# Performance work log

Measured on AMD Instinct MI355X. Metric: run time of the kernel, lower is better.

## Reference

```python
import jax, jax.numpy as jnp
import numpy as np

BSZ, L, D = 8, 2048, 1024

def setup_inputs() -> dict:
    key = jax.random.key(0)
    k1, k2, k3, k4 = jax.random.split(key, 4)
    s = 1.0 / np.sqrt(D)
    return {
        "x":   jax.random.normal(k1, (BSZ, L, D), dtype=jnp.float32),
        "A":   jax.random.normal(k2, (D,), dtype=jnp.float32),
        "W_B": jax.random.normal(k3, (D, D), dtype=jnp.float32) * s,
        "b_B": jnp.zeros((D,), dtype=jnp.float32),
        "W_C": jax.random.normal(k4, (D, D), dtype=jnp.float32) * s,
        "b_C": jnp.zeros((D,), dtype=jnp.float32),
    }

def reference(x, A, W_B, b_B, W_C, b_C):
    # Precompute B(x_t) for all t in one GEMM: [B, L, D]
    Bx = jnp.einsum("bld,ed->ble", x, W_B) + b_B
    h0 = jnp.zeros((x.shape[0], x.shape[2]), dtype=x.dtype)

    def step(h, bx_t):
        h = jnp.tanh(A * h + bx_t)   # elementwise recurrence
        return h, h

    # scan over time: Bx -> [L, B, D]
    _, hs = jax.lax.scan(step, h0, jnp.swapaxes(Bx, 0, 1))
    # y_t = C(h_t), batched over all t: hs [L, B, D]
    y = jnp.einsum("lbd,ed->lbe", hs, W_C) + b_C
    return jnp.swapaxes(y, 0, 1)  # [B, L, D]
```

## Files before the change

### kernel.cpp

```cpp
#include <hip/hip_runtime.h>
#include <hip/hip_bf16.h>
#include <stdint.h>


using short8 = __attribute__((ext_vector_type(8))) short;
using f32x4  = __attribute__((ext_vector_type(4))) float;

#define DEV __device__ __forceinline__

DEV ushort f2bf_rn(float x) {
  uint32_t u = __float_as_uint(x);
  uint32_t r = (u + 0x7FFFu + ((u >> 16) & 1u)) >> 16;
  return (ushort)r;
}
DEV float bf2f(ushort b) { return __uint_as_float(((uint32_t)b) << 16); }

DEV void gload_lds16(const void* g, void* l) {
  __builtin_amdgcn_global_load_lds((const __attribute__((address_space(1))) void*)g,
                                   (__attribute__((address_space(3))) void*)l,
                                   16, 0, 0);
}

__global__ void k_split_convert(const float* __restrict__ in, ushort* __restrict__ hi,
                                ushort* __restrict__ lo, int n4) {
  const int stride = gridDim.x * blockDim.x;
  for (int i = blockIdx.x * blockDim.x + threadIdx.x; i < n4; i += stride) {
    float4 v = reinterpret_cast<const float4*>(in)[i];
    ushort4 hv, lv;
    hv.x = f2bf_rn(v.x); lv.x = f2bf_rn(v.x - bf2f(hv.x));
    hv.y = f2bf_rn(v.y); lv.y = f2bf_rn(v.y - bf2f(hv.y));
    hv.z = f2bf_rn(v.z); lv.z = f2bf_rn(v.z - bf2f(hv.z));
    hv.w = f2bf_rn(v.w); lv.w = f2bf_rn(v.w - bf2f(hv.w));
    reinterpret_cast<ushort4*>(hi)[i] = hv;
    reinterpret_cast<ushort4*>(lo)[i] = lv;
  }
}

__global__ void k_convert(const float* __restrict__ in, ushort* __restrict__ hi, int n4) {
  const int stride = gridDim.x * blockDim.x;
  for (int i = blockIdx.x * blockDim.x + threadIdx.x; i < n4; i += stride) {
    float4 v = reinterpret_cast<const float4*>(in)[i];
    ushort4 hv;
    hv.x = f2bf_rn(v.x); hv.y = f2bf_rn(v.y);
    hv.z = f2bf_rn(v.z); hv.w = f2bf_rn(v.w);
    reinterpret_cast<ushort4*>(hi)[i] = hv;
  }
}

template <int SPLIT>
__global__ __launch_bounds__(256, 2)
void k_gemm_bt(const ushort* __restrict__ Ah, const ushort* __restrict__ Al,
               const ushort* __restrict__ Bh, const ushort* __restrict__ Bl,
               const float* __restrict__ bias, float* __restrict__ C,
               int M, int N, int K) {
  constexpr int NMAT = SPLIT ? 4 : 2;
  __shared__ __align__(1024) ushort lds[NMAT * 128 * 64];
  ushort* sAh = lds;
  ushort* sAl = lds + (SPLIT ? 8192 : 0);
  ushort* sBh = lds + (SPLIT ? 16384 : 8192);
  ushort* sBl = lds + (SPLIT ? 24576 : 8192);

  const int t = threadIdx.x;
  const int lane = t & 63;
  const int w = t >> 6;
  const int wm = w >> 1, wn = w & 1;
  const int bm = blockIdx.y, bn = blockIdx.x;
  const int lr = lane & 15;
  const int lk = (lane >> 4) << 3;

  const ushort* gA_h = Ah + (size_t)(bm * 128) * K;
  const ushort* gA_l = SPLIT ? (Al + (size_t)(bm * 128) * K) : gA_h;
  const ushort* gB_h = Bh + (size_t)(bn * 128) * K;
  const ushort* gB_l = SPLIT ? (Bl + (size_t)(bn * 128) * K) : gB_h;

  f32x4 acc[4][4];
#pragma unroll
  for (int i = 0; i < 4; ++i)
#pragma unroll
    for (int j = 0; j < 4; ++j)
#pragma unroll
      for (int r = 0; r < 4; ++r) acc[i][j][r] = 0.f;

  auto stage = [&](int kt) {
    const int k0 = kt * 64;
#pragma unroll
    for (int i = 0; i < 4; ++i) {
      const int lin16 = i * 256 + t;
      const int lb = lin16 << 4;
      const int row = lb >> 7;
      const int srcb = (lb & 127) ^ ((row & 7) << 4);
      const size_t goff = (size_t)row * K + (size_t)(k0 + (srcb >> 1));
      const int lidx = i * 2048 + w * 512;
      gload_lds16(gA_h + goff, sAh + lidx);
      if (SPLIT) gload_lds16(gA_l + goff, sAl + lidx);
      gload_lds16(gB_h + goff, sBh + lidx);
      if (SPLIT) gload_lds16(gB_l + goff, sBl + lidx);
    }
  };

  auto ldfrag = [&](const ushort* s, int row, int kc) -> short8 {
    const int byte = (row << 7) + (((kc << 1) ^ ((row & 7) << 4)));
    return *reinterpret_cast<const short8*>(reinterpret_cast<const char*>(s) + byte);
  };

  const int NT = K / 64;
  stage(0);
  for (int kt = 0; kt < NT; ++kt) {
    __syncthreads();
#pragma unroll
    for (int kk = 0; kk < 2; ++kk) {
      short8 ah[4], bh[4], al[4], bl[4];
      const int kc = kk * 32 + lk;
#pragma unroll
      for (int i = 0; i < 4; ++i) {
        const int row = wm * 64 + i * 16 + lr;
        ah[i] = ldfrag(sAh, row, kc);
        if (SPLIT) al[i] = ldfrag(sAl, row, kc);
      }
#pragma unroll
      for (int j = 0; j < 4; ++j) {
        const int row = wn * 64 + j * 16 + lr;
        bh[j] = ldfrag(sBh, row, kc);
        if (SPLIT) bl[j] = ldfrag(sBl, row, kc);
      }
#pragma unroll
      for (int i = 0; i < 4; ++i)
#pragma unroll
        for (int j = 0; j < 4; ++j) {
          acc[i][j] = __builtin_amdgcn_mfma_f32_16x16x32_bf16(ah[i], bh[j], acc[i][j], 0, 0, 0);
          if (SPLIT) {
            acc[i][j] = __builtin_amdgcn_mfma_f32_16x16x32_bf16(al[i], bh[j], acc[i][j], 0, 0, 0);
            acc[i][j] = __builtin_amdgcn_mfma_f32_16x16x32_bf16(ah[i], bl[j], acc[i][j], 0, 0, 0);
          }
        }
    }
    __syncthreads();
    if (kt + 1 < NT) stage(kt + 1);
  }

  float* Cb = C + (size_t)(bm * 128) * N + bn * 128;
#pragma unroll
  for (int i = 0; i < 4; ++i)
#pragma unroll
    for (int j = 0; j < 4; ++j) {
      const int col = wn * 64 + j * 16 + lr;
      const float bv = bias[bn * 128 + col];
#pragma unroll
      for (int r = 0; r < 4; ++r) {
        const int rowt = wm * 64 + i * 16 + ((lane >> 4) << 2) + r;
        Cb[(size_t)rowt * N + col] = acc[i][j][r] + bv;
      }
    }
}

__global__ __launch_bounds__(64)
void k_recurrence(const float* __restrict__ Bx, const float* __restrict__ Avec,
                  ushort* __restrict__ Hout) {
  const int tid = blockIdx.x * 64 + threadIdx.x;
  const int b = tid >> 10;
  const int d = tid & 1023;
  const float a = Avec[d];
  const float* bx = Bx + (size_t)b * 2048 * 1024 + d;
  ushort* ho = Hout + (size_t)b * 2048 * 1024 + d;

  constexpr int P = 32;
  constexpr int NC = 2048 / P;
  float buf[P];
#pragma unroll
  for (int i = 0; i < P; ++i) buf[i] = bx[(size_t)i * 1024];
  float h = 0.f;
  for (int c = 0; c < NC; ++c) {
    float nbuf[P];
    if (c + 1 < NC) {
#pragma unroll
      for (int i = 0; i < P; ++i) nbuf[i] = bx[(size_t)((c + 1) * P + i) * 1024];
    } else {
#pragma unroll
      for (int i = 0; i < P; ++i) nbuf[i] = 0.f;
    }
#pragma unroll
    for (int i = 0; i < P; ++i) {
      float u = fmaf(a, h, buf[i]);
      u = fminf(15.f, fmaxf(-15.f, u));
      const float p = __expf(u + u);
      h = (p - 1.f) * __builtin_amdgcn_rcpf(p + 1.f);
      ho[(size_t)(c * P + i) * 1024] = f2bf_rn(h);
    }
#pragma unroll
    for (int i = 0; i < P; ++i) buf[i] = nbuf[i];
  }
}

extern "C" void kernel_launch(void* const* d_in, const int* in_sizes, int n_in,
                              void* d_out, int out_size, void* d_ws, size_t ws_size,
                              hipStream_t stream) {
  const float* x   = (const float*)d_in[0];
  const float* A   = (const float*)d_in[1];
  const float* W_B = (const float*)d_in[2];
  const float* b_B = (const float*)d_in[3];
  const float* W_C = (const float*)d_in[4];
  const float* b_C = (const float*)d_in[5];
  float* y = (float*)d_out;

  const int Bsz = 8, L = 2048, D = 1024;
  const int M = Bsz * L;

  char* ws = (char*)d_ws;
  ushort* x_hi  = (ushort*)(ws);
  ushort* x_lo  = (ushort*)(ws + 33554432);
  ushort* wb_hi = (ushort*)(ws + 67108864);
  ushort* wb_lo = (ushort*)(ws + 69206016);
  ushort* wc_h  = (ushort*)(ws + 71303168);
  float*  Bx    = (float*)(ws + 73400320);
  ushort* h     = x_hi;

  k_split_convert<<<2048, 256, 0, stream>>>(x, x_hi, x_lo, M * D / 4);
  k_split_convert<<<1024, 256, 0, stream>>>(W_B, wb_hi, wb_lo, D * D / 4);
  k_convert<<<1024, 256, 0, stream>>>(W_C, wc_h, D * D / 4);

  k_gemm_bt<1><<<dim3(D / 128, M / 128), 256, 0, stream>>>(
      x_hi, x_lo, wb_hi, wb_lo, b_B, Bx, M, D, D);

  k_recurrence<<<(Bsz * D) / 64, 64, 0, stream>>>(Bx, A, h);

  k_gemm_bt<0><<<dim3(D / 128, M / 128), 256, 0, stream>>>(
      h, (const ushort*)nullptr, wc_h, (const ushort*)nullptr, b_C, y, M, D, D);
}
```

Baseline: 286.0 us.

## Switch GEMMs to fp16, XCD-aware tile remap, and streamline tanh recurrence

Swaps the bf16 hi/lo split and MFMA for fp16, which gives more mantissa bits, and stores h in fp16. Adds an XCD-aware remapping of block indices so neighbouring M tiles share an XCD's L2. Folds the 2·log2(e) scaling into the first GEMM's epilogue, so the recurrence computes tanh with exp2, one rcp and one fma and drops the clamp. The recurrence also double-buffers its Bx loads in two register banks. Risks include fp16 overflow or inf in exp2 without the clamp, which rcp should still handle, and more register pressure in the recurrence.

```diff
diff --git a/kernel.cpp b/kernel.cpp
--- a/kernel.cpp
+++ b/kernel.cpp
@@ -3,17 +3,29 @@
 #include <stdint.h>
 
 
-using short8 = __attribute__((ext_vector_type(8))) short;
-using f32x4  = __attribute__((ext_vector_type(4))) float;
+using half8 = __attribute__((ext_vector_type(8))) _Float16;
+using f32x4 = __attribute__((ext_vector_type(4))) float;
 
 #define DEV __device__ __forceinline__
 
-DEV ushort f2bf_rn(float x) {
-  uint32_t u = __float_as_uint(x);
-  uint32_t r = (u + 0x7FFFu + ((u >> 16) & 1u)) >> 16;
-  return (ushort)r;
-}
-DEV float bf2f(ushort b) { return __uint_as_float(((uint32_t)b) << 16); }
+#if __has_builtin(__builtin_amdgcn_exp2f)
+DEV float pexp(float x) { return __builtin_amdgcn_exp2f(x); }
+constexpr float BX_SCALE = 2.8853900817779268f;
+#else
+DEV float pexp(float x) { return __expf(x); }
+constexpr float BX_SCALE = 2.0f;
+#endif
+
+DEV ushort f2h(float x) {
+  union { _Float16 f; ushort u; } c;
+  c.f = (_Float16)x;
+  return c.u;
+}
+DEV float h2f(ushort u) {
+  union { ushort u; _Float16 f; } c;
+  c.u = u;
+  return (float)c.f;
+}
 
 DEV void gload_lds16(const void* g, void* l) {
   __builtin_amdgcn_global_load_lds((const __attribute__((address_space(1))) void*)g,
@@ -27,27 +39,27 @@
   for (int i = blockIdx.x * blockDim.x + threadIdx.x; i < n4; i += stride) {
     float4 v = reinterpret_cast<const float4*>(in)[i];
     ushort4 hv, lv;
-    hv.x = f2bf_rn(v.x); lv.x = f2bf_rn(v.x - bf2f(hv.x));
-    hv.y = f2bf_rn(v.y); lv.y = f2bf_rn(v.y - bf2f(hv.y));
-    hv.z = f2bf_rn(v.z); lv.z = f2bf_rn(v.z - bf2f(hv.z));
-    hv.w = f2bf_rn(v.w); lv.w = f2bf_rn(v.w - bf2f(hv.w));
+    hv.x = f2h(v.x); lv.x = f2h(v.x - h2f(hv.x));
+    hv.y = f2h(v.y); lv.y = f2h(v.y - h2f(hv.y));
+    hv.z = f2h(v.z); lv.z = f2h(v.z - h2f(hv.z));
+    hv.w = f2h(v.w); lv.w = f2h(v.w - h2f(hv.w));
     reinterpret_cast<ushort4*>(hi)[i] = hv;
     reinterpret_cast<ushort4*>(lo)[i] = lv;
   }
 }
 
-__global__ void k_convert(const float* __restrict__ in, ushort* __restrict__ hi, int n4) {
+__global__ void k_convert(const float* __restrict__ in, ushort* __restrict__ out, int n4) {
   const int stride = gridDim.x * blockDim.x;
   for (int i = blockIdx.x * blockDim.x + threadIdx.x; i < n4; i += stride) {
     float4 v = reinterpret_cast<const float4*>(in)[i];
     ushort4 hv;
-    hv.x = f2bf_rn(v.x); hv.y = f2bf_rn(v.y);
-    hv.z = f2bf_rn(v.z); hv.w = f2bf_rn(v.w);
-    reinterpret_cast<ushort4*>(hi)[i] = hv;
-  }
-}
-
-template <int SPLIT>
+    hv.x = f2h(v.x); hv.y = f2h(v.y);
+    hv.z = f2h(v.z); hv.w = f2h(v.w);
+    reinterpret_cast<ushort4*>(out)[i] = hv;
+  }
+}
+
+template <int SPLIT, int SCALE>
 __global__ __launch_bounds__(256, 2)
 void k_gemm_bt(const ushort* __restrict__ Ah, const ushort* __restrict__ Al,
                const ushort* __restrict__ Bh, const ushort* __restrict__ Bl,
@@ -64,7 +76,17 @@
   const int lane = t & 63;
   const int w = t >> 6;
   const int wm = w >> 1, wn = w & 1;
-  const int bm = blockIdx.y, bn = blockIdx.x;
+
+  int bm, bn;
+  if (gridDim.x == 8) {
+    const int l = blockIdx.y * 8 + blockIdx.x;
+    const int xcd = l & 7, s = l >> 3;
+    bm = ((s >> 3) << 3) | xcd;
+    bn = s & 7;
+  } else {
+    bm = blockIdx.y; bn = blockIdx.x;
+  }
+
   const int lr = lane & 15;
   const int lk = (lane >> 4) << 3;
 
@@ -98,9 +120,9 @@
     }
   };
 
-  auto ldfrag = [&](const ushort* s, int row, int kc) -> short8 {
+  auto ldfrag = [&](const ushort* s, int row, int kc) -> half8 {
     const int byte = (row << 7) + (((kc << 1) ^ ((row & 7) << 4)));
-    return *reinterpret_cast<const short8*>(reinterpret_cast<const char*>(s) + byte);
+    return *reinterpret_cast<const half8*>(reinterpret_cast<const char*>(s) + byte);
   };
 
   const int NT = K / 64;
@@ -109,7 +131,7 @@
     __syncthreads();
 #pragma unroll
     for (int kk = 0; kk < 2; ++kk) {
-      short8 ah[4], bh[4], al[4], bl[4];
+      half8 ah[4], bh[4], al[4], bl[4];
       const int kc = kk * 32 + lk;
 #pragma unroll
       for (int i = 0; i < 4; ++i) {
@@ -127,10 +149,10 @@
       for (int i = 0; i < 4; ++i)
 #pragma unroll
         for (int j = 0; j < 4; ++j) {
-          acc[i][j] = __builtin_amdgcn_mfma_f32_16x16x32_bf16(ah[i], bh[j], acc[i][j], 0, 0, 0);
+          acc[i][j] = __builtin_amdgcn_mfma_f32_16x16x32_f16(ah[i], bh[j], acc[i][j], 0, 0, 0);
           if (SPLIT) {
-            acc[i][j] = __builtin_amdgcn_mfma_f32_16x16x32_bf16(al[i], bh[j], acc[i][j], 0, 0, 0);
-            acc[i][j] = __builtin_amdgcn_mfma_f32_16x16x32_bf16(ah[i], bl[j], acc[i][j], 0, 0, 0);
+            acc[i][j] = __builtin_amdgcn_mfma_f32_16x16x32_f16(al[i], bh[j], acc[i][j], 0, 0, 0);
+            acc[i][j] = __builtin_amdgcn_mfma_f32_16x16x32_f16(ah[i], bl[j], acc[i][j], 0, 0, 0);
           }
         }
     }
@@ -148,46 +170,57 @@
 #pragma unroll
       for (int r = 0; r < 4; ++r) {
         const int rowt = wm * 64 + i * 16 + ((lane >> 4) << 2) + r;
-        Cb[(size_t)rowt * N + col] = acc[i][j][r] + bv;
+        float o = acc[i][j][r] + bv;
+        if (SCALE) o *= BX_SCALE;
+        Cb[(size_t)rowt * N + col] = o;
       }
     }
 }
 
 __global__ __launch_bounds__(64)
-void k_recurrence(const float* __restrict__ Bx, const float* __restrict__ Avec,
+void k_recurrence(const float* __restrict__ Bx2, const float* __restrict__ Avec,
                   ushort* __restrict__ Hout) {
   const int tid = blockIdx.x * 64 + threadIdx.x;
   const int b = tid >> 10;
   const int d = tid & 1023;
-  const float a = Avec[d];
-  const float* bx = Bx + (size_t)b * 2048 * 1024 + d;
+  const float a2 = BX_SCALE * Avec[d];
+  const float* bx = Bx2 + (size_t)b * 2048 * 1024 + d;
   ushort* ho = Hout + (size_t)b * 2048 * 1024 + d;
 
   constexpr int P = 32;
   constexpr int NC = 2048 / P;
-  float buf[P];
-#pragma unroll
-  for (int i = 0; i < P; ++i) buf[i] = bx[(size_t)i * 1024];
+  float bufA[P], bufB[P];
+#pragma unroll
+  for (int i = 0; i < P; ++i) bufA[i] = bx[(size_t)i * 1024];
+#pragma unroll
+  for (int i = 0; i < P; ++i) bufB[i] = bx[(size_t)(P + i) * 1024];
+
   float h = 0.f;
-  for (int c = 0; c < NC; ++c) {
-    float nbuf[P];
-    if (c + 1 < NC) {
-#pragma unroll
-      for (int i = 0; i < P; ++i) nbuf[i] = bx[(size_t)((c + 1) * P + i) * 1024];
-    } else {
-#pragma unroll
-      for (int i = 0; i < P; ++i) nbuf[i] = 0.f;
-    }
+  for (int c = 0; c < NC; c += 2) {
 #pragma unroll
     for (int i = 0; i < P; ++i) {
-      float u = fmaf(a, h, buf[i]);
-      u = fminf(15.f, fmaxf(-15.f, u));
-      const float p = __expf(u + u);
-      h = (p - 1.f) * __builtin_amdgcn_rcpf(p + 1.f);
-      ho[(size_t)(c * P + i) * 1024] = f2bf_rn(h);
-    }
-#pragma unroll
-    for (int i = 0; i < P; ++i) buf[i] = nbuf[i];
+      const float u2 = fmaf(a2, h, bufA[i]);
+      const float p  = pexp(u2);
+      const float r  = __builtin_amdgcn_rcpf(p + 1.f);
+      h = fmaf(-2.f, r, 1.f);
+      ho[(size_t)(c * P + i) * 1024] = f2h(h);
+    }
+    if (c + 2 < NC) {
+#pragma unroll
+      for (int i = 0; i < P; ++i) bufA[i] = bx[(size_t)((c + 2) * P + i) * 1024];
+    }
+#pragma unroll
+    for (int i = 0; i < P; ++i) {
+      const float u2 = fmaf(a2, h, bufB[i]);
+      const float p  = pexp(u2);
+      const float r  = __builtin_amdgcn_rcpf(p + 1.f);
+      h = fmaf(-2.f, r, 1.f);
+      ho[(size_t)((c + 1) * P + i) * 1024] = f2h(h);
+    }
+    if (c + 3 < NC) {
+#pragma unroll
+      for (int i = 0; i < P; ++i) bufB[i] = bx[(size_t)((c + 3) * P + i) * 1024];
+    }
   }
 }
 
@@ -210,19 +243,19 @@
   ushort* x_lo  = (ushort*)(ws + 33554432);
   ushort* wb_hi = (ushort*)(ws + 67108864);
   ushort* wb_lo = (ushort*)(ws + 69206016);
-  ushort* wc_h  = (ushort*)(ws + 71303168);
+  ushort* wc    = (ushort*)(ws + 71303168);
   float*  Bx    = (float*)(ws + 73400320);
   ushort* h     = x_hi;
 
   k_split_convert<<<2048, 256, 0, stream>>>(x, x_hi, x_lo, M * D / 4);
-  k_split_convert<<<1024, 256, 0, stream>>>(W_B, wb_hi, wb_lo, D * D / 4);
-  k_convert<<<1024, 256, 0, stream>>>(W_C, wc_h, D * D / 4);
-
-  k_gemm_bt<1><<<dim3(D / 128, M / 128), 256, 0, stream>>>(
+  k_split_convert<<<512, 256, 0, stream>>>(W_B, wb_hi, wb_lo, D * D / 4);
+  k_convert<<<512, 256, 0, stream>>>(W_C, wc, D * D / 4);
+
+  k_gemm_bt<1, 1><<<dim3(D / 128, M / 128), 256, 0, stream>>>(
       x_hi, x_lo, wb_hi, wb_lo, b_B, Bx, M, D, D);
 
   k_recurrence<<<(Bsz * D) / 64, 64, 0, stream>>>(Bx, A, h);
 
-  k_gemm_bt<0><<<dim3(D / 128, M / 128), 256, 0, stream>>>(
-      h, (const ushort*)nullptr, wc_h, (const ushort*)nullptr, b_C, y, M, D, D);
-}
+  k_gemm_bt<0, 0><<<dim3(D / 128, M / 128), 256, 0, stream>>>(
+      h, (const ushort*)nullptr, wc, (const ushort*)nullptr, b_C, y, M, D, D);
+}
```

Result: faster. 232.6 us (-18.7%).
